# Kernel tuning notes

Measured on AMD Instinct MI355X. Metric: run time of the kernel, lower is better.

Reference implementation:

```python
import jax, jax.numpy as jnp
import numpy as np

K = 1024  # num_codebook_vectors
D = 256   # latent_dim


def setup_inputs() -> dict:
    key = jax.random.key(0)
    k1, k2 = jax.random.split(key)
    z = jax.random.normal(k1, (16, D, 64, 64), dtype=jnp.float32)
    # nn.Embedding weight init: uniform(-1/K, 1/K)
    emb_weight = jax.random.uniform(k2, (K, D), dtype=jnp.float32,
                                    minval=-1.0 / K, maxval=1.0 / K)
    return {"z": z, "emb_weight": emb_weight}


def reference(z, emb_weight):
    B, C, H, W = z.shape  # C == D
    # NCHW -> NHWC, flatten to [N, D]
    z_nhwc = jnp.transpose(z, (0, 2, 3, 1))
    zf = z_nhwc.reshape(-1, C)  # [N, D]
    # squared L2 distances: ||z||^2 + ||e||^2 - 2 z e^T
    d = (jnp.sum(zf * zf, axis=1, keepdims=True)
         + jnp.sum(emb_weight * emb_weight, axis=1)
         - 2.0 * jnp.einsum('nd,kd->nk', zf, emb_weight))  # [N, K]
    min_encoding_indices = jnp.argmin(d, axis=1)  # [N] int
    z_q = emb_weight[min_encoding_indices].reshape(B, H, W, C)
    z_q = jnp.transpose(z_q, (0, 3, 1, 2))  # back to NCHW
    return (min_encoding_indices, z_q)
```

## Files before the change

### kernel.cpp

```cpp
#include <hip/hip_runtime.h>
#include <hip/hip_bf16.h>
#include <stdint.h>
#include <stddef.h>

typedef __attribute__((ext_vector_type(4))) float f32x4;
typedef _Float16 f16x8 __attribute__((ext_vector_type(8)));
typedef _Float16 f16x4 __attribute__((ext_vector_type(4)));

#define BN 128
#define MARGIN 230.0f

__device__ float g_embn[1024];

__global__ __launch_bounds__(256) void emb_prep_kernel(const float* __restrict__ emb,
                                                       _Float16* __restrict__ embf) {
    int row = blockIdx.x * 4 + (threadIdx.x >> 6);
    int l   = threadIdx.x & 63;
    f32x4 v = *(const f32x4*)&emb[(size_t)row * 256 + l * 4];
    f16x4 h;
    float s = 0.f;
#pragma unroll
    for (int j = 0; j < 4; ++j) {
        h[j] = (_Float16)(v[j] * 1024.0f);
        float f = (float)h[j];
        s = fmaf(f, f, s);
    }
    *(f16x4*)&embf[(size_t)row * 256 + l * 4] = h;
#pragma unroll
    for (int off = 1; off < 64; off <<= 1) s += __shfl_xor(s, off, 64);
    if (l == 0) g_embn[row] = s;
}

__device__ __forceinline__ void prefetch_B(const _Float16* __restrict__ embf,
                                           _Float16* bbuf, int s, int t) {
    int kt = s >> 3, ds = s & 7;
    int code = t >> 2;
    int slot = t & 3;
    int g    = (slot ^ code ^ (code >> 2)) & 3;
    const _Float16* src = embf + (((size_t)(kt * 128 + code)) << 8) + ds * 32 + g * 8;
    void* dst = (void*)(bbuf + (size_t)t * 8);
    __builtin_amdgcn_global_load_lds((const __attribute__((address_space(1))) void*)src,
                                     (__attribute__((address_space(3))) void*)dst,
                                     16, 0, 0);
}

__global__ __launch_bounds__(512, 4) void vq_kernel(
        const float* __restrict__ z,
        const float* __restrict__ emb,
        const _Float16* __restrict__ embf,
        float* __restrict__ out) {

    __shared__ _Float16 A_sh[BN * 256];
    __shared__ _Float16 B_sh[2][BN * 32];

    const int t  = threadIdx.x;
    const int w  = t >> 6;
    const int l  = t & 63;
    const int c  = l & 15;
    const int q  = l >> 4;
    const int wr = w >> 1;
    const int wc = w & 1;

    const int n0    = blockIdx.x * BN;
    const int b_img = n0 >> 12;
    const int hw0   = n0 & 4095;
    const float* zb = z + (size_t)b_img * (256 * 4096) + hw0;

#pragma unroll
    for (int it = 0; it < 2; ++it) {
        int task = it * 512 + t;
        int nq = task & 31;
        int dg = task >> 5;
        const float* g = zb + (size_t)(dg * 8) * 4096 + nq * 4;
        f32x4 col[8];
#pragma unroll
        for (int j = 0; j < 8; ++j) col[j] = *(const f32x4*)(g + (size_t)j * 4096);
#pragma unroll
        for (int u = 0; u < 4; ++u) {
            int n = nq * 4 + u;
            f16x8 v;
#pragma unroll
            for (int j = 0; j < 8; ++j) v[j] = (_Float16)col[j][u];
            *(f16x8*)&A_sh[n * 256 + ((dg ^ (n & 7)) * 8)] = v;
        }
    }
    __syncthreads();

    prefetch_B(embf, &B_sh[0][0], 0, t);

    f32x4 acc[2][4];
    float v1[8], v2[8];
    int   i1[8], i2[8];
#pragma unroll
    for (int i = 0; i < 2; ++i)
#pragma unroll
        for (int j = 0; j < 4; ++j) acc[i][j] = (f32x4){0.f, 0.f, 0.f, 0.f};
#pragma unroll
    for (int p = 0; p < 8; ++p) { v1[p] = 3.4e38f; v2[p] = 3.4e38f; i1[p] = 0x7fffffff; i2[p] = 0x7fffffff; }

    for (int kt = 0; kt < 8; ++kt) {
        float en4[4];
#pragma unroll
        for (int j = 0; j < 4; ++j) en4[j] = g_embn[kt * 128 + wc * 64 + j * 16 + c];

#pragma unroll
        for (int ds = 0; ds < 8; ++ds) {
            int s = kt * 8 + ds;
            __syncthreads();
            if (s + 1 < 64) prefetch_B(embf, &B_sh[(s + 1) & 1][0], s + 1, t);

            const _Float16* Bb = &B_sh[s & 1][0];

            f16x8 af[2], bfr[4];
#pragma unroll
            for (int i = 0; i < 2; ++i) {
                int n  = wr * 32 + i * 16 + c;
                int pg = ((ds << 2) + q) ^ (n & 7);
                af[i] = *(const f16x8*)&A_sh[n * 256 + pg * 8];
            }
#pragma unroll
            for (int j = 0; j < 4; ++j) {
                int k = wc * 64 + j * 16 + c;
                bfr[j] = *(const f16x8*)&Bb[k * 32 + (((q ^ k ^ (k >> 2)) & 3) * 8)];
            }
#pragma unroll
            for (int i = 0; i < 2; ++i)
#pragma unroll
                for (int j = 0; j < 4; ++j)
                    acc[i][j] = __builtin_amdgcn_mfma_f32_16x16x32_f16(af[i], bfr[j], acc[i][j], 0, 0, 0);
        }

#pragma unroll
        for (int j = 0; j < 4; ++j) {
            float en = en4[j];
            int code = kt * 128 + wc * 64 + j * 16 + c;
#pragma unroll
            for (int i = 0; i < 2; ++i) {
#pragma unroll
                for (int r = 0; r < 4; ++r) {
                    int p = i * 4 + r;
                    float sc = fmaf(-2048.0f, acc[i][j][r], en);
                    if (sc < v1[p]) {
                        v2[p] = v1[p]; i2[p] = i1[p];
                        v1[p] = sc;    i1[p] = code;
                    } else if (sc < v2[p]) {
                        v2[p] = sc;    i2[p] = code;
                    }
                }
            }
        }
#pragma unroll
        for (int i = 0; i < 2; ++i)
#pragma unroll
            for (int j = 0; j < 4; ++j) acc[i][j] = (f32x4){0.f, 0.f, 0.f, 0.f};
    }

    __syncthreads();

    float* cv = (float*)A_sh;
    int*   ci = ((int*)A_sh) + 8192;
    int* idx_fin = (int*)&B_sh[0][0];
    int* wl_n    = idx_fin + 128;
    int* wl_row  = idx_fin + 129;
    int* wl_nc   = idx_fin + 257;
    int* wl_cand = idx_fin + 385;

    if (t == 0) wl_n[0] = 0;
#pragma unroll
    for (int p = 0; p < 8; ++p) {
        int row = wr * 32 + (p >> 2) * 16 + q * 4 + (p & 3);
        int s0  = (wc * 16 + c) * 2;
        cv[s0 * 128       + ((row + s0)     & 127)] = v1[p];
        ci[s0 * 128       + ((row + s0)     & 127)] = i1[p];
        cv[(s0 + 1) * 128 + ((row + s0 + 1) & 127)] = v2[p];
        ci[(s0 + 1) * 128 + ((row + s0 + 1) & 127)] = i2[p];
    }
    __syncthreads();

    if (t < BN) {
        float mv = 3.4e38f; int mi = 0x7fffffff;
#pragma unroll 8
        for (int s = 0; s < 64; ++s) {
            float v = cv[s * 128 + ((t + s) & 127)];
            int  id = ci[s * 128 + ((t + s) & 127)];
            if (v < mv || (v == mv && id < mi)) { mv = v; mi = id; }
        }
        int   cand[8]; int nc = 0;
        float thr = mv + MARGIN;
        for (int s = 0; s < 64; ++s) {
            float v = cv[s * 128 + ((t + s) & 127)];
            int  id = ci[s * 128 + ((t + s) & 127)];
            if (v <= thr && id < 1024 && nc < 8) cand[nc++] = id;
        }
        idx_fin[t] = mi;
        if (nc > 1) {
            int slot = atomicAdd(wl_n, 1);
            wl_row[slot] = t;
            wl_nc[slot]  = nc;
            for (int i = 0; i < nc; ++i) wl_cand[slot * 8 + i] = cand[i];
        }
    }
    __syncthreads();

    int nwl = wl_n[0];
    for (int e = w; e < nwl; e += 8) {
        int row = wl_row[e];
        int nc  = wl_nc[e];
        const float* zrow = zb + row;

        int j  = l & 15, h = j >> 3, jj = j & 7;
        float x0 = zrow[(size_t)(h * 128 + jj) * 4096];
        float r  = __fmul_rn(x0, x0);
        for (int m = 1; m < 16; ++m) {
            float x = zrow[(size_t)(h * 128 + jj + 8 * m) * 4096];
            r = __fadd_rn(r, __fmul_rn(x, x));
        }
        float s1 = __fadd_rn(r,  __shfl_xor(r,  1, 64));
        float s2 = __fadd_rn(s1, __shfl_xor(s1, 2, 64));
        float s4 = __fadd_rn(s2, __shfl_xor(s2, 4, 64));
        float a_n = __fadd_rn(s4, __shfl_xor(s4, 8, 64));
        a_n = __shfl(a_n, 0, 64);

        float best = 3.4e38f; int bid = 0x7fffffff;
        for (int cx = 0; cx < nc; ++cx) {
            int id = wl_cand[e * 8 + cx];
            const float* er = emb + (size_t)id * 256;
            float y0 = er[h * 128 + jj];
            float rb = __fmul_rn(y0, y0);
            for (int m = 1; m < 16; ++m) {
                float y = er[h * 128 + jj + 8 * m];
                rb = __fadd_rn(rb, __fmul_rn(y, y));
            }
            float b1 = __fadd_rn(rb, __shfl_xor(rb, 1, 64));
            float b2 = __fadd_rn(b1, __shfl_xor(b1, 2, 64));
            float b4 = __fadd_rn(b2, __shfl_xor(b2, 4, 64));
            float b_k = __fadd_rn(b4, __shfl_xor(b4, 8, 64));
            b_k = __shfl(b_k, 0, 64);
            double cd = 0.0;
#pragma unroll
            for (int u = 0; u < 4; ++u) {
                int d = l + u * 64;
                cd = fma((double)zrow[(size_t)d * 4096], (double)er[d], cd);
            }
#pragma unroll
            for (int off = 1; off < 64; off <<= 1) cd += __shfl_xor(cd, off, 64);
            float c32 = (float)cd;
            float sc  = __fsub_rn(__fadd_rn(a_n, b_k), __fmul_rn(2.0f, c32));
            if (sc < best || (sc == best && id < bid)) { best = sc; bid = id; }
        }
        if (l == 0) idx_fin[row] = bid;
    }
    __syncthreads();

    if (t < BN) out[n0 + t] = (float)idx_fin[t];

    float* zq = out + 65536 + (size_t)b_img * (256 * 4096) + hw0;
    {
        int m   = t & 127;
        int sub = t >> 7;
        int id  = idx_fin[m];
        const float* er = emb + (size_t)id * 256;
#pragma unroll 4
        for (int it = 0; it < 16; ++it) {
            int d4 = it * 4 + sub;
            f32x4 v = *(const f32x4*)&er[d4 * 4];
#pragma unroll
            for (int jj2 = 0; jj2 < 4; ++jj2)
                zq[(size_t)(d4 * 4 + jj2) * 4096 + m] = v[jj2];
        }
    }
}

extern "C" void kernel_launch(void* const* d_in, const int* in_sizes, int n_in,
                              void* d_out, int out_size, void* d_ws, size_t ws_size,
                              hipStream_t stream) {
    const float* z   = (const float*)d_in[0];
    const float* emb = (const float*)d_in[1];
    _Float16* embf = (_Float16*)d_ws;
    float* out = (float*)d_out;

    emb_prep_kernel<<<256, 256, 0, stream>>>(emb, embf);
    vq_kernel<<<65536 / BN, 512, 0, stream>>>(z, emb, embf, out);
}
```

Baseline: 187.9 us.

## Pre-pack codebook in MFMA fragment order and load B directly to registers

The prep kernel now writes the fp16 codebook in the exact per-lane MFMA fragment order. The main kernel then loads B fragments straight from global memory (L2-resident) into double-buffered registers instead of staging them through LDS with global_load_lds and a barrier every step. This removes one __syncthreads per k-step along with the LDS traffic for B. In exchange, every wave issues its own global loads, so each of the 4 row-waves re-reads the same data, and register pressure rises. The A swizzle also changes to reduce bank conflicts.

```diff
diff --git a/kernel.cpp b/kernel.cpp
--- a/kernel.cpp
+++ b/kernel.cpp
@@ -5,43 +5,40 @@
 
 typedef __attribute__((ext_vector_type(4))) float f32x4;
 typedef _Float16 f16x8 __attribute__((ext_vector_type(8)));
-typedef _Float16 f16x4 __attribute__((ext_vector_type(4)));
 
 #define BN 128
 #define MARGIN 230.0f
 
 __device__ float g_embn[1024];
 
+__device__ __forceinline__ int swzA(int n) { return (n ^ (n >> 3)) & 7; }
+
 __global__ __launch_bounds__(256) void emb_prep_kernel(const float* __restrict__ emb,
                                                        _Float16* __restrict__ embf) {
-    int row = blockIdx.x * 4 + (threadIdx.x >> 6);
-    int l   = threadIdx.x & 63;
-    f32x4 v = *(const f32x4*)&emb[(size_t)row * 256 + l * 4];
-    f16x4 h;
+    int tid  = blockIdx.x * 256 + threadIdx.x;
+    int code = tid >> 5;
+    int g8   = tid & 31;
+    const float* src = emb + (size_t)code * 256 + g8 * 8;
+    f32x4 v0 = *(const f32x4*)src;
+    f32x4 v1 = *(const f32x4*)(src + 4);
+    f16x8 h;
     float s = 0.f;
 #pragma unroll
     for (int j = 0; j < 4; ++j) {
-        h[j] = (_Float16)(v[j] * 1024.0f);
-        float f = (float)h[j];
-        s = fmaf(f, f, s);
-    }
-    *(f16x4*)&embf[(size_t)row * 256 + l * 4] = h;
-#pragma unroll
-    for (int off = 1; off < 64; off <<= 1) s += __shfl_xor(s, off, 64);
-    if (l == 0) g_embn[row] = s;
-}
-
-__device__ __forceinline__ void prefetch_B(const _Float16* __restrict__ embf,
-                                           _Float16* bbuf, int s, int t) {
-    int kt = s >> 3, ds = s & 7;
-    int code = t >> 2;
-    int slot = t & 3;
-    int g    = (slot ^ code ^ (code >> 2)) & 3;
-    const _Float16* src = embf + (((size_t)(kt * 128 + code)) << 8) + ds * 32 + g * 8;
-    void* dst = (void*)(bbuf + (size_t)t * 8);
-    __builtin_amdgcn_global_load_lds((const __attribute__((address_space(1))) void*)src,
-                                     (__attribute__((address_space(3))) void*)dst,
-                                     16, 0, 0);
+        h[j]     = (_Float16)(v0[j] * 1024.0f);
+        h[4 + j] = (_Float16)(v1[j] * 1024.0f);
+        float a = (float)h[j], b = (float)h[4 + j];
+        s = fmaf(a, a, s); s = fmaf(b, b, s);
+    }
+#pragma unroll
+    for (int off = 1; off < 32; off <<= 1) s += __shfl_xor(s, off, 64);
+    if (g8 == 0) g_embn[code] = s;
+
+    int kt = code >> 7, r = code & 127;
+    int wc = r >> 6, j4 = (r >> 4) & 3, c = r & 15;
+    int ds = g8 >> 2, q = g8 & 3, l = q * 16 + c;
+    size_t off16 = ((((size_t)(kt * 8 + ds) * 2 + wc) * 4 + j4) * 64 + l) * 8;
+    *(f16x8*)&embf[off16] = h;
 }
 
 __global__ __launch_bounds__(512, 4) void vq_kernel(
@@ -51,7 +48,7 @@
         float* __restrict__ out) {
 
     __shared__ _Float16 A_sh[BN * 256];
-    __shared__ _Float16 B_sh[2][BN * 32];
+    __shared__ int      W_sh[1410];
 
     const int t  = threadIdx.x;
     const int w  = t >> 6;
@@ -81,12 +78,12 @@
             f16x8 v;
 #pragma unroll
             for (int j = 0; j < 8; ++j) v[j] = (_Float16)col[j][u];
-            *(f16x8*)&A_sh[n * 256 + ((dg ^ (n & 7)) * 8)] = v;
-        }
-    }
-    __syncthreads();
-
-    prefetch_B(embf, &B_sh[0][0], 0, t);
+            *(f16x8*)&A_sh[n * 256 + ((dg ^ swzA(n)) * 8)] = v;
+        }
+    }
+    __syncthreads();
+
+    const char* bbase = (const char*)embf + ((size_t)wc << 12) + ((size_t)l << 4);
 
     f32x4 acc[2][4];
     float v1[8], v2[8];
@@ -98,6 +95,11 @@
 #pragma unroll
     for (int p = 0; p < 8; ++p) { v1[p] = 3.4e38f; v2[p] = 3.4e38f; i1[p] = 0x7fffffff; i2[p] = 0x7fffffff; }
 
+    f16x8 bb[2][4];
+#pragma unroll
+    for (int j = 0; j < 4; ++j)
+        bb[0][j] = *(const f16x8*)(bbase + j * 1024);
+
     for (int kt = 0; kt < 8; ++kt) {
         float en4[4];
 #pragma unroll
@@ -105,29 +107,26 @@
 
 #pragma unroll
         for (int ds = 0; ds < 8; ++ds) {
-            int s = kt * 8 + ds;
-            __syncthreads();
-            if (s + 1 < 64) prefetch_B(embf, &B_sh[(s + 1) & 1][0], s + 1, t);
-
-            const _Float16* Bb = &B_sh[s & 1][0];
-
-            f16x8 af[2], bfr[4];
+            const int s   = kt * 8 + ds;
+            const int cur = ds & 1, nxt = cur ^ 1;
+            if (ds < 7 || kt < 7) {
+                const char* np = bbase + (size_t)(s + 1) * 8192;
+#pragma unroll
+                for (int j = 0; j < 4; ++j)
+                    bb[nxt][j] = *(const f16x8*)(np + j * 1024);
+            }
+            f16x8 af[2];
 #pragma unroll
             for (int i = 0; i < 2; ++i) {
                 int n  = wr * 32 + i * 16 + c;
-                int pg = ((ds << 2) + q) ^ (n & 7);
+                int pg = ((ds << 2) + q) ^ swzA(n);
                 af[i] = *(const f16x8*)&A_sh[n * 256 + pg * 8];
             }
 #pragma unroll
-            for (int j = 0; j < 4; ++j) {
-                int k = wc * 64 + j * 16 + c;
-                bfr[j] = *(const f16x8*)&Bb[k * 32 + (((q ^ k ^ (k >> 2)) & 3) * 8)];
-            }
-#pragma unroll
             for (int i = 0; i < 2; ++i)
 #pragma unroll
                 for (int j = 0; j < 4; ++j)
-                    acc[i][j] = __builtin_amdgcn_mfma_f32_16x16x32_f16(af[i], bfr[j], acc[i][j], 0, 0, 0);
+                    acc[i][j] = __builtin_amdgcn_mfma_f32_16x16x32_f16(af[i], bb[cur][j], acc[i][j], 0, 0, 0);
         }
 
 #pragma unroll
@@ -159,11 +158,11 @@
 
     float* cv = (float*)A_sh;
     int*   ci = ((int*)A_sh) + 8192;
-    int* idx_fin = (int*)&B_sh[0][0];
-    int* wl_n    = idx_fin + 128;
-    int* wl_row  = idx_fin + 129;
-    int* wl_nc   = idx_fin + 257;
-    int* wl_cand = idx_fin + 385;
+    int* idx_fin = W_sh;
+    int* wl_n    = W_sh + 128;
+    int* wl_row  = W_sh + 129;
+    int* wl_nc   = W_sh + 257;
+    int* wl_cand = W_sh + 385;
 
     if (t == 0) wl_n[0] = 0;
 #pragma unroll
@@ -279,6 +278,6 @@
     _Float16* embf = (_Float16*)d_ws;
     float* out = (float*)d_out;
 
-    emb_prep_kernel<<<256, 256, 0, stream>>>(emb, embf);
+    emb_prep_kernel<<<128, 256, 0, stream>>>(emb, embf);
     vq_kernel<<<65536 / BN, 512, 0, stream>>>(z, emb, embf, out);
 }
```

Measured after the change: 360.3 us. 91.7% more time.
